# Performance work log

Hardware: AMD Instinct MI355X
Metric: run time of the kernel (lower is better)

The kernel has to match this reference:

```python
import jax, jax.numpy as jnp
import numpy as np
from jax import lax

B, C, H, W = 32, 3, 128, 128
S = 10             # max_segments
L = 200            # base_traj_length
TOTAL_LIMIT = 200  # traj_length (must equal L per original sample())
DOF = 2
HID = 2048
CONV_OUT = 512 * 6 * 6  # 128->126->63->61->30->28->14->12->6


def _conv(x, w, b):
    y = lax.conv_general_dilated(x, w, (1, 1), 'VALID', dimension_numbers=('NCHW', 'OIHW', 'NCHW'))
    return y + b[None, :, None, None]


def _pool_relu(x):
    return jax.nn.relu(lax.reduce_window(x, -jnp.inf, lax.max, (1, 1, 2, 2), (1, 1, 2, 2), 'VALID'))


def _rotate2d(y, y0, rot):
    # rotate points y (B,L,2) around per-batch center y0 (B,2) by rot (B,1,1) radians
    px, py = y[..., 0:1], y[..., 1:2]
    cx, cy = y0[:, 0][:, None, None], y0[:, 1][:, None, None]
    c, s = jnp.cos(rot), jnp.sin(rot)
    return jnp.concatenate([c * (px - cx) - s * (py - cy) + cx,
                            s * (px - cx) + c * (py - cy) + cy], axis=2)


def _sample(traj, ratio):
    b, T = traj.shape[0], traj.shape[1]
    f32 = traj.dtype
    seg_limit = jnp.ceil(ratio * TOTAL_LIMIT)  # (B,S)
    # redistribution: shave 1 off the (first) max segment while over budget.
    # original runs over_limit.max() iterations; over_limit <= S-1, extras are no-ops (still_over gate).
    for _ in range(S):
        max_val = seg_limit.max(axis=1)
        still_over = (seg_limit.sum(axis=1) != float(L)).astype(f32)
        reduced = jnp.ones((b,), f32)
        for j in range(S):
            mult = jnp.abs(jnp.sign(max_val - seg_limit[:, j]) - 1.0)
            seg_limit = seg_limit.at[:, j].add(-mult * reduced * still_over)
            reduced = jnp.clip(reduced - mult, 0.0)
    seg_ids = np.arange(T) // L
    # replicates original condition: i>0 and cur_segment_idx != floor(i - 1/L)  (note: i - 1/L, as written)
    forces = np.array([(i > 0) and (seg_ids[i] != int(np.floor(i - 1.0 / L))) for i in range(T)])
    di0 = jnp.floor((L - 1.0) / seg_limit[:, 0:1])
    init = (di0, jnp.zeros((b, 1), f32), jnp.zeros((b, 1), f32), jnp.zeros((b, S), f32))

    def step(state, inp):
        di, last_idx, n_tot, seg_cnt = state
        i_f, seg, force = inp
        lim = lax.dynamic_index_in_dim(seg_limit, seg, axis=1, keepdims=True)  # (B,1)
        cnt = lax.dynamic_index_in_dim(seg_cnt, seg, axis=1, keepdims=True)    # (B,1)
        new_di = jnp.floor((L - 1.0 - (last_idx - seg.astype(f32) * L)) / (lim - cnt))
        di = jnp.where(force | (di < new_di), new_di, di)
        chk = (jnp.sign(jnp.clip(TOTAL_LIMIT - n_tot, 0.0))
               * (cnt < lim).astype(f32)
               * (i_f - last_idx == di).astype(f32))
        last_idx = jnp.maximum(last_idx, i_f * chk)
        seg_cnt = lax.dynamic_update_index_in_dim(seg_cnt, (cnt + chk)[:, 0], seg, axis=1)
        return (di, last_idx, n_tot + chk, seg_cnt), chk[:, 0]

    xs = (jnp.arange(T, dtype=f32), jnp.asarray(seg_ids, jnp.int32), jnp.asarray(forces))
    _, mask_t = lax.scan(step, init, xs)
    mask = mask_t.T > 0  # (B,T) velocity mask; exactly TOTAL_LIMIT true per row
    idx = jnp.argsort(jnp.where(mask, 0, 1), axis=1)[:, :TOTAL_LIMIT]  # stable sort -> ordered true positions
    return jnp.take_along_axis(traj, idx[:, :, None], axis=1)


def _forward(x, w1, b1, w2, b2, w3, b3, w4, b4, fcw1, fcb1, fcw2, fcb2,
             wi, bi, ws, bs, wr, br, base_traj):
    h = _pool_relu(_conv(x, w1, b1))
    h = _pool_relu(_conv(h, w2, b2))
    h = _pool_relu(_conv(h, w3, b3))
    h = _pool_relu(_conv(h, w4, b4))
    feat = h.reshape(h.shape[0], -1)  # (B, CONV_OUT)
    z = jnp.tanh(feat @ fcw1.T + fcb1)
    z = z @ fcw2.T + fcb2             # dropout == identity (eval mode)
    init_pos = z @ wi.T + bi                                   # (B,DOF)
    seg_mod = (z @ ws.T + bs).reshape(z.shape[0], S, DOF + 1)  # (B,S,DOF+1)
    ratio = jax.nn.softmax(z @ wr.T + br, axis=1)              # (B,S)
    last_pos = init_pos[:, None, :]
    starts, segs = [last_pos], []
    for i in range(S):
        scaling = seg_mod[:, i, :-1]
        rot = jnp.tanh(seg_mod[:, i, -1])[:, None, None] * 3.14
        m = base_traj * scaling[:, None, :]
        m = _rotate2d(m, m[:, 0, :], rot)
        m = last_pos + m
        last_pos = m[:, -1:, :]
        starts.append(last_pos)
        segs.append(m)
    traj = jnp.concatenate(segs, axis=1)             # (B,S*L,DOF) unsampled
    seg_start_end = jnp.concatenate(starts, axis=1)  # (B,S+1,DOF)
    sampled = _sample(traj, ratio)                   # (B,TOTAL_LIMIT,DOF)
    return sampled, seg_start_end, ratio, traj


def setup_inputs():
    key = jax.random.key(0)
    ks = jax.random.split(key, 12)
    n = lambda k, s, sc: jax.random.normal(k, s, jnp.float32) * sc
    t = jnp.linspace(0.0, 1.0, L)
    base_traj = jnp.stack([t, jnp.sin(t * jnp.pi)], axis=-1)[None]  # (1,L,2)
    return {
        'x': n(ks[0], (B, C, H, W), 1.0),
        'w1': n(ks[1], (64, C, 3, 3), 0.05), 'b1': jnp.zeros((64,), jnp.float32),
        'w2': n(ks[2], (128, 64, 3, 3), 0.05), 'b2': jnp.zeros((128,), jnp.float32),
        'w3': n(ks[3], (256, 128, 3, 3), 0.05), 'b3': jnp.zeros((256,), jnp.float32),
        'w4': n(ks[4], (512, 256, 3, 3), 0.05), 'b4': jnp.zeros((512,), jnp.float32),
        'fcw1': n(ks[5], (HID, CONV_OUT), 0.01), 'fcb1': jnp.zeros((HID,), jnp.float32),
        'fcw2': n(ks[6], (HID, HID), 0.02), 'fcb2': jnp.zeros((HID,), jnp.float32),
        'wi': n(ks[7], (DOF, HID), 0.02), 'bi': jnp.zeros((DOF,), jnp.float32),
        'ws': n(ks[8], (S * (DOF + 1), HID), 0.02), 'bs': jnp.zeros((S * (DOF + 1),), jnp.float32),
        'wr': n(ks[9], (S, HID), 0.05), 'br': jnp.zeros((S,), jnp.float32),
        'base_traj': base_traj,
    }


def reference(x, w1, b1, w2, b2, w3, b3, w4, b4, fcw1, fcb1, fcw2, fcb2,
              wi, bi, ws, bs, wr, br, base_traj):
    return _forward(x, w1, b1, w2, b2, w3, b3, w4, b4, fcw1, fcb1, fcw2, fcb2,
                    wi, bi, ws, bs, wr, br, base_traj)
```

## Files before the change

kernel.cpp:

```cpp
#include <hip/hip_runtime.h>

__global__ __launch_bounds__(256)
void conv1_lds(const float* __restrict__ in, const float* __restrict__ wt,
               const float* __restrict__ bias, float* __restrict__ out)
{
    __shared__ float sh[3][34][34];
    int bx = blockIdx.x;
    int tile = bx & 15;
    int cg   = (bx >> 4) & 7;
    int b    = bx >> 7;
    int tr = tile >> 2, tc = tile & 3;
    int tid = threadIdx.x;
    int ty = tid >> 4, tx = tid & 15;
    int R0 = 32 * tr, C0 = 32 * tc;

    for (int t = tid; t < 3 * 34 * 34; t += 256) {
        int ci = t / 1156;
        int rem = t - ci * 1156;
        int rr = rem / 34, cc = rem - rr * 34;
        int gr = R0 + rr; if (gr > 127) gr = 127;
        int gc = C0 + cc; if (gc > 127) gc = 127;
        sh[ci][rr][cc] = in[(((size_t)b * 3 + ci) * 128 + gr) * 128 + gc];
    }
    __syncthreads();

    float acc[8][2][2] = {};
    int co0 = cg * 8;
#pragma unroll
    for (int ci = 0; ci < 3; ++ci) {
        float p[4][4];
#pragma unroll
        for (int r = 0; r < 4; ++r) {
            const float2* pr = reinterpret_cast<const float2*>(&sh[ci][2 * ty + r][2 * tx]);
            float2 a = pr[0], c2 = pr[1];
            p[r][0] = a.x; p[r][1] = a.y; p[r][2] = c2.x; p[r][3] = c2.y;
        }
#pragma unroll
        for (int j = 0; j < 8; ++j) {
            const float* wj = wt + ((size_t)(co0 + j) * 3 + ci) * 9;
#pragma unroll
            for (int kh = 0; kh < 3; ++kh)
#pragma unroll
                for (int kw = 0; kw < 3; ++kw) {
                    float wv = wj[kh * 3 + kw];
#pragma unroll
                    for (int dy = 0; dy < 2; ++dy)
#pragma unroll
                        for (int dx = 0; dx < 2; ++dx)
                            acc[j][dy][dx] = fmaf(wv, p[dy + kh][dx + kw], acc[j][dy][dx]);
                }
        }
    }
    int py = 16 * tr + ty, px = 16 * tc + tx;
    if (py < 63 && px < 63) {
#pragma unroll
        for (int j = 0; j < 8; ++j) {
            float v = fmaxf(fmaxf(acc[j][0][0], acc[j][0][1]),
                            fmaxf(acc[j][1][0], acc[j][1][1])) + bias[co0 + j];
            out[(((size_t)b * 64 + co0 + j) * 63 + py) * 63 + px] = fmaxf(v, 0.f);
        }
    }
}

template<int CIN, int DIM, int POOL, int COUT, int TILES_R, int TILES_C>
__global__ __launch_bounds__(256)
void conv_v7(const float* __restrict__ in, const float* __restrict__ wt,
             const float* __restrict__ bias, float* __restrict__ out)
{
    __shared__ __align__(16) float sh[4 * 18 * 36];
    __shared__ float wsh[16 * 37];

    constexpr int NT  = TILES_R * TILES_C;
    constexpr int NCG = COUT / 16;
    int bx = blockIdx.x;
    int tile = bx % NT;
    int cg   = (bx / NT) % NCG;
    int b    = bx / (NT * NCG);
    int rt = tile / TILES_C, ct = tile % TILES_C;
    int tid = threadIdx.x;
    int co_l = tid & 15;
    int sp   = tid >> 4;
    int ty = sp >> 2, tx = sp & 3;
    int co = cg * 16 + co_l;
    int R0 = 16 * rt, C0 = 32 * ct;

    int gofs[10], lofs[10];
#pragma unroll
    for (int j = 0; j < 10; ++j) {
        int t = tid + 256 * j; if (t > 2447) t = 2447;
        int ci = t / 612;
        int rem = t - ci * 612;
        int rr = rem / 34, cc = rem - rr * 34;
        int gr = R0 + rr; if (gr > DIM - 1) gr = DIM - 1;
        int gc = C0 + cc; if (gc > DIM - 1) gc = DIM - 1;
        gofs[j] = ci * DIM * DIM + gr * DIM + gc;
        lofs[j] = ci * 648 + rr * 36 + cc;
    }
    int wgofs[3], wlofs[3];
#pragma unroll
    for (int j = 0; j < 3; ++j) {
        int t = tid + 256 * j; if (t > 575) t = 575;
        int c = t / 36, q = t - c * 36;
        wgofs[j] = (cg * 16 + c) * CIN * 9 + q;
        wlofs[j] = c * 37 + q;
    }

    const float* gbase = in + (size_t)b * CIN * DIM * DIM;

    float acc[4][8] = {};
    float sr[10], wr[3];

#pragma unroll
    for (int j = 0; j < 10; ++j) sr[j] = gbase[gofs[j]];
#pragma unroll
    for (int j = 0; j < 3; ++j) wr[j] = wt[wgofs[j]];

    constexpr int ITERS = CIN / 4;
    for (int it = 0; it < ITERS; ++it) {
#pragma unroll
        for (int j = 0; j < 10; ++j) sh[lofs[j]] = sr[j];
#pragma unroll
        for (int j = 0; j < 3; ++j) wsh[wlofs[j]] = wr[j];
        __syncthreads();
        if (it < ITERS - 1) {
            const float* gn = gbase + (size_t)(it + 1) * 4 * DIM * DIM;
#pragma unroll
            for (int j = 0; j < 10; ++j) sr[j] = gn[gofs[j]];
            const float* wn = wt + (it + 1) * 36;
#pragma unroll
            for (int j = 0; j < 3; ++j) wr[j] = wn[wgofs[j]];
        }
#pragma unroll
        for (int ci = 0; ci < 4; ++ci) {
            float w[9];
#pragma unroll
            for (int k = 0; k < 9; ++k) w[k] = wsh[co_l * 37 + ci * 9 + k];
            const float* rb = sh + ci * 648 + 8 * tx;
#pragma unroll
            for (int r = 0; r < 6; ++r) {
                const float* rp = rb + (4 * ty + r) * 36;
                float4 a = *reinterpret_cast<const float4*>(rp);
                float4 b4 = *reinterpret_cast<const float4*>(rp + 4);
                float2 c2 = *reinterpret_cast<const float2*>(rp + 8);
                float row[10];
                row[0] = a.x;  row[1] = a.y;  row[2] = a.z;  row[3] = a.w;
                row[4] = b4.x; row[5] = b4.y; row[6] = b4.z; row[7] = b4.w;
                row[8] = c2.x; row[9] = c2.y;
#pragma unroll
                for (int y = 0; y < 4; ++y) {
                    if (y < r - 2 || y > r) continue;
                    int kh = r - y;
#pragma unroll
                    for (int kw = 0; kw < 3; ++kw) {
                        float wv = w[kh * 3 + kw];
#pragma unroll
                        for (int x = 0; x < 8; ++x)
                            acc[y][x] = fmaf(wv, row[x + kw], acc[y][x]);
                    }
                }
            }
        }
        __syncthreads();
    }
    float bz = bias[co];
#pragma unroll
    for (int dy = 0; dy < 2; ++dy) {
        int py = 8 * rt + 2 * ty + dy;
#pragma unroll
        for (int dx = 0; dx < 4; ++dx) {
            int px = 16 * ct + 4 * tx + dx;
            if (py < POOL && px < POOL) {
                float v = fmaxf(fmaxf(acc[2 * dy][2 * dx],     acc[2 * dy][2 * dx + 1]),
                                fmaxf(acc[2 * dy + 1][2 * dx], acc[2 * dy + 1][2 * dx + 1]));
                out[(((size_t)b * COUT + co) * POOL + py) * POOL + px] = fmaxf(v + bz, 0.f);
            }
        }
    }
}

__global__ __launch_bounds__(256)
void conv4_v3(const float* __restrict__ in, const float* __restrict__ wt,
              const float* __restrict__ bias, float* __restrict__ out)
{
    __shared__ __align__(16) float smem[4032 + 4 * 16 * 37];
    float* in_sh = smem;
    float* w_sh  = smem + 4032;
    float* red   = smem;

    int bx = blockIdx.x;
    int cg = bx & 31;
    int b  = bx >> 5;
    int tid = threadIdx.x;
    int h   = tid >> 6;
    int r6  = tid & 63;
    int cog = r6 >> 3;
    int sub = r6 & 7;
    int R = 3 * (sub >> 1), C = 6 * (sub & 1);

    float acc[2][3][6] = {};
    float sin_r[13];
    float sw_r[9];

    const size_t in_b = (size_t)b * 256 * 196;

#pragma unroll
    for (int j = 0; j < 13; ++j) {
        int g = tid + 256 * j;
        if (g < 3136) {
            int hh = g / 784, rem = g - hh * 784;
            int ci = rem / 196, r2 = rem - ci * 196;
            sin_r[j] = in[in_b + (size_t)(hh * 64 + ci) * 196 + r2];
        }
    }
#pragma unroll
    for (int j = 0; j < 9; ++j) {
        int g = tid + 256 * j;
        int hh = g / 576, rem = g - hh * 576;
        int co = rem / 36, q = rem - co * 36;
        sw_r[j] = wt[(size_t)(cg * 16 + co) * 2304 + (size_t)(hh * 64) * 9 + q];
    }

    for (int it = 0; it < 16; ++it) {
#pragma unroll
        for (int j = 0; j < 13; ++j) {
            int g = tid + 256 * j;
            if (g < 3136) {
                int hh = g / 784, rem = g - hh * 784;
                int ci = rem / 196, r2 = rem - ci * 196;
                int rr = r2 / 14, cc = r2 - rr * 14;
                in_sh[((hh * 4 + ci) * 14 + rr) * 18 + cc] = sin_r[j];
            }
        }
#pragma unroll
        for (int j = 0; j < 9; ++j) {
            int g = tid + 256 * j;
            int hh = g / 576, rem = g - hh * 576;
            int co = rem / 36, q = rem - co * 36;
            w_sh[(hh * 16 + co) * 37 + q] = sw_r[j];
        }
        __syncthreads();
        if (it < 15) {
            int k0n = (it + 1) * 4;
#pragma unroll
            for (int j = 0; j < 13; ++j) {
                int g = tid + 256 * j;
                if (g < 3136) {
                    int hh = g / 784, rem = g - hh * 784;
                    int ci = rem / 196, r2 = rem - ci * 196;
                    sin_r[j] = in[in_b + (size_t)(hh * 64 + k0n + ci) * 196 + r2];
                }
            }
#pragma unroll
            for (int j = 0; j < 9; ++j) {
                int g = tid + 256 * j;
                int hh = g / 576, rem = g - hh * 576;
                int co = rem / 36, q = rem - co * 36;
                sw_r[j] = wt[(size_t)(cg * 16 + co) * 2304 + (size_t)(hh * 64 + k0n) * 9 + q];
            }
        }
#pragma unroll
        for (int ci = 0; ci < 4; ++ci) {
            float w[2][9];
#pragma unroll
            for (int c = 0; c < 2; ++c)
#pragma unroll
                for (int k = 0; k < 9; ++k)
                    w[c][k] = w_sh[(h * 16 + 2 * cog + c) * 37 + ci * 9 + k];
            const float* rowbase = in_sh + ((h * 4 + ci) * 14) * 18;
#pragma unroll
            for (int r = 0; r < 5; ++r) {
                float row[8];
                const float2* pr = reinterpret_cast<const float2*>(rowbase + (size_t)(R + r) * 18 + C);
                float2 a0 = pr[0], a1 = pr[1], a2 = pr[2], a3 = pr[3];
                row[0] = a0.x; row[1] = a0.y; row[2] = a1.x; row[3] = a1.y;
                row[4] = a2.x; row[5] = a2.y; row[6] = a3.x; row[7] = a3.y;
#pragma unroll
                for (int y = 0; y < 3; ++y) {
                    if (y < r - 2 || y > r) continue;
                    int kh = r - y;
#pragma unroll
                    for (int c = 0; c < 2; ++c)
#pragma unroll
                        for (int kw = 0; kw < 3; ++kw) {
                            float wv = w[c][kh * 3 + kw];
#pragma unroll
                            for (int x = 0; x < 6; ++x)
                                acc[c][y][x] = fmaf(wv, row[x + kw], acc[c][y][x]);
                        }
                }
            }
        }
        __syncthreads();
    }
#pragma unroll
    for (int hh = 0; hh < 4; ++hh) {
        if (h == hh) {
#pragma unroll
            for (int c = 0; c < 2; ++c)
#pragma unroll
                for (int y = 0; y < 3; ++y)
#pragma unroll
                    for (int x = 0; x < 6; ++x) {
                        float* dst = &red[((2 * cog + c) * 12 + R + y) * 13 + C + x];
                        if (hh == 0) *dst = acc[c][y][x];
                        else         *dst += acc[c][y][x];
                    }
        }
        __syncthreads();
    }
    for (int t = tid; t < 576; t += 256) {
        int co = t / 36, rem = t - co * 36;
        int pr = rem / 6, pc = rem - pr * 6;
        const float* rp = &red[(co * 12 + 2 * pr) * 13 + 2 * pc];
        float v = fmaxf(fmaxf(rp[0], rp[1]), fmaxf(rp[13], rp[14]));
        v += bias[cg * 16 + co];
        out[(((size_t)b * 512 + cg * 16 + co) * 6 + pr) * 6 + pc] = fmaxf(v, 0.f);
    }
}

__global__ __launch_bounds__(1024)
void fc_big(const float* __restrict__ X, const float* __restrict__ W,
            const float* __restrict__ bias, float* __restrict__ Y,
            int K, int N, int act)
{
    __shared__ float red[32][32][8];
    int o0 = blockIdx.x * 8;
    int s = threadIdx.x & 31;
    int b = threadIdx.x >> 5;
    int K4 = K >> 2;
    const float4* X4 = reinterpret_cast<const float4*>(X) + (size_t)b * K4;
    const float4* W4 = reinterpret_cast<const float4*>(W);

    float acc[8] = {};
    for (int k4 = s; k4 < K4; k4 += 32) {
        float4 xv = X4[k4];
#pragma unroll
        for (int o = 0; o < 8; ++o) {
            float4 wv = W4[(size_t)(o0 + o) * K4 + k4];
            acc[o] = fmaf(xv.x, wv.x,
                     fmaf(xv.y, wv.y,
                     fmaf(xv.z, wv.z,
                     fmaf(xv.w, wv.w, acc[o]))));
        }
    }
#pragma unroll
    for (int o = 0; o < 8; ++o) red[b][s][o] = acc[o];
    __syncthreads();
    if (threadIdx.x < 256) {
        int bb = threadIdx.x >> 3, oo = threadIdx.x & 7;
        float v = bias[o0 + oo];
#pragma unroll 8
        for (int ss = 0; ss < 32; ++ss) v += red[bb][ss][oo];
        if (act) v = tanhf(v);
        Y[(size_t)bb * N + o0 + oo] = v;
    }
}

__global__ __launch_bounds__(256)
void fc_two(const float* __restrict__ X, const float* __restrict__ W,
            const float* __restrict__ bias, float* __restrict__ Y,
            int K, int N, int act)
{
    int o0 = blockIdx.x * 2;
    int tid = threadIdx.x;
    const float* w0 = W + (size_t)o0 * K;
    const float* w1 = w0 + K;
    float a0[32], a1[32];
#pragma unroll
    for (int b = 0; b < 32; ++b) { a0[b] = 0.f; a1[b] = 0.f; }

    for (int k = tid; k < K; k += 256) {
        float wv0 = w0[k], wv1 = w1[k];
#pragma unroll
        for (int b = 0; b < 32; ++b) {
            float xv = X[(size_t)b * K + k];
            a0[b] = fmaf(wv0, xv, a0[b]);
            a1[b] = fmaf(wv1, xv, a1[b]);
        }
    }
    __shared__ float part[2][4][32];
    int lane = tid & 63, wv = tid >> 6;
#pragma unroll
    for (int b = 0; b < 32; ++b) {
        float s0 = a0[b], s1 = a1[b];
#pragma unroll
        for (int off = 32; off >= 1; off >>= 1) {
            s0 += __shfl_down(s0, off);
            s1 += __shfl_down(s1, off);
        }
        if (lane == 0) { part[0][wv][b] = s0; part[1][wv][b] = s1; }
    }
    __syncthreads();
    if (tid < 64) {
        int j = tid >> 5, b = tid & 31;
        float s = part[j][0][b] + part[j][1][b] + part[j][2][b] + part[j][3][b] + bias[o0 + j];
        if (act) s = tanhf(s);
        Y[(size_t)b * N + o0 + j] = s;
    }
}

__global__ __launch_bounds__(64)
void post_kernel(const float* __restrict__ logits, float* __restrict__ ratio_out,
                 float* __restrict__ sl_out)
{
    int b = threadIdx.x;
    if (b >= 32) return;
    float lg[10];
#pragma unroll
    for (int j = 0; j < 10; ++j) lg[j] = logits[b * 10 + j];
    float mx = lg[0];
#pragma unroll
    for (int j = 1; j < 10; ++j) mx = fmaxf(mx, lg[j]);
    float e[10]; float ssum = 0.f;
#pragma unroll
    for (int j = 0; j < 10; ++j) { e[j] = expf(lg[j] - mx); ssum += e[j]; }
    float sl[10];
#pragma unroll
    for (int j = 0; j < 10; ++j) {
        float r = e[j] / ssum;
        ratio_out[b * 10 + j] = r;
        sl[j] = ceilf(r * 200.f);
    }
#pragma unroll
    for (int it = 0; it < 10; ++it) {
        float s = 0.f, mx2 = sl[0];
#pragma unroll
        for (int j = 0; j < 10; ++j) { s += sl[j]; mx2 = fmaxf(mx2, sl[j]); }
        float over = (s != 200.f) ? 1.f : 0.f;
        float reduced = 1.f;
#pragma unroll
        for (int j = 0; j < 10; ++j) {
            float mult = (sl[j] == mx2) ? 1.f : 0.f;
            sl[j] -= mult * reduced * over;
            reduced = fmaxf(reduced - mult, 0.f);
        }
    }
#pragma unroll
    for (int j = 0; j < 10; ++j) sl_out[b * 10 + j] = sl[j];
}

__global__ __launch_bounds__(256)
void traj_kernel(const float* __restrict__ base, const float* __restrict__ ipos,
                 const float* __restrict__ sm, float* __restrict__ out_traj,
                 float* __restrict__ out_starts)
{
    int b = blockIdx.x;
    int j = threadIdx.x;
    float bx0 = base[0], by0 = base[1];
    float bxL = base[398], byL = base[399];
    float bx = 0.f, by = 0.f;
    if (j < 200) { bx = base[2 * j]; by = base[2 * j + 1]; }
    float curx = ipos[b * 2 + 0], cury = ipos[b * 2 + 1];
    if (j == 0) { out_starts[b * 22 + 0] = curx; out_starts[b * 22 + 1] = cury; }
#pragma unroll
    for (int i = 0; i < 10; ++i) {
        float sx  = sm[b * 30 + i * 3 + 0];
        float sy  = sm[b * 30 + i * 3 + 1];
        float rot = tanhf(sm[b * 30 + i * 3 + 2]) * 3.14f;
        float c = cosf(rot), s = sinf(rot);
        float cx = bx0 * sx, cy = by0 * sy;
        if (j < 200) {
            float px = bx * sx, py = by * sy;
            float rx = c * (px - cx) - s * (py - cy) + cx;
            float ry = s * (px - cx) + c * (py - cy) + cy;
            size_t o = ((size_t)b * 2000 + i * 200 + j) * 2;
            out_traj[o + 0] = curx + rx;
            out_traj[o + 1] = cury + ry;
        }
        float pxL = bxL * sx, pyL = byL * sy;
        float exL = c * (pxL - cx) - s * (pyL - cy) + cx;
        float eyL = s * (pxL - cx) + c * (pyL - cy) + cy;
        curx += exL; cury += eyL;
        if (j == 0) {
            out_starts[b * 22 + (i + 1) * 2 + 0] = curx;
            out_starts[b * 22 + (i + 1) * 2 + 1] = cury;
        }
    }
}

__global__ __launch_bounds__(64)
void sample_kernel(const float* __restrict__ sl_in, const float* __restrict__ traj,
                   float* __restrict__ samp_out)
{
    __shared__ unsigned int maskb[32][63];
    __shared__ float ssl[32][10];
    int tid = threadIdx.x;
    for (int t = tid; t < 32 * 63; t += 64) ((unsigned int*)maskb)[t] = 0u;
    for (int t = tid; t < 32 * 10; t += 64) ((float*)ssl)[t] = sl_in[t];
    __syncthreads();
    if (tid >= 32) return;
    int b = tid;
    const float* tb = traj + (size_t)b * 4000;
    float* sp = samp_out + (size_t)b * 400;
    int out_n = 0;
    float last = 0.f, ntot = 0.f;
    float lim0 = ssl[b][0];
    float di = floorf(199.f / lim0);
    float ct0 = 0.f;
    if ((ntot < 200.f) && (ct0 < lim0) && (0.f - last == di)) {
        ntot += 1.f; ct0 += 1.f;
        maskb[b][0] |= 1u;
        sp[out_n * 2] = tb[0]; sp[out_n * 2 + 1] = tb[1]; ++out_n;
    }
    {
        float ndi = floorf((199.f - last) / (lim0 - ct0));
        if (di < ndi) di = ndi;
        if ((ntot < 200.f) && (ct0 < lim0) && (1.f - last == di)) {
            last = 1.f; ntot += 1.f; ct0 += 1.f;
            maskb[b][0] |= 2u;
            sp[out_n * 2] = tb[2]; sp[out_n * 2 + 1] = tb[3]; ++out_n;
        }
    }
    for (int seg = 0; seg < 10; ++seg) {
        float lim = ssl[b][seg];
        float ct = (seg == 0) ? ct0 : 0.f;
        float segbase = 200.f * seg;
        float segend = segbase + 199.f;
        float pos = (seg == 0) ? 2.f : segbase;
        float ndi = floorf((199.f - (last - segbase)) / (lim - ct));
        while ((ntot < 200.f) && (ct < lim)) {
            float fi = last + ndi;
            if (!(fi >= pos && fi <= segend)) break;
            int i = (int)fi;
            last = fi; ntot += 1.f; ct += 1.f;
            maskb[b][i >> 5] |= (1u << (i & 31));
            sp[out_n * 2] = tb[2 * i]; sp[out_n * 2 + 1] = tb[2 * i + 1]; ++out_n;
            pos = fi + 1.f;
            ndi = floorf((199.f - (last - segbase)) / (lim - ct));
        }
    }
    for (int i = 0; i < 2000 && out_n < 200; ++i) {
        if (!((maskb[b][i >> 5] >> (i & 31)) & 1u)) {
            sp[out_n * 2] = tb[2 * i]; sp[out_n * 2 + 1] = tb[2 * i + 1]; ++out_n;
        }
    }
}

extern "C" void kernel_launch(void* const* d_in, const int* in_sizes, int n_in,
                              void* d_out, int out_size, void* d_ws, size_t ws_size,
                              hipStream_t stream)
{
    const float* x    = (const float*)d_in[0];
    const float* w1   = (const float*)d_in[1];
    const float* b1   = (const float*)d_in[2];
    const float* w2   = (const float*)d_in[3];
    const float* b2   = (const float*)d_in[4];
    const float* w3   = (const float*)d_in[5];
    const float* b3   = (const float*)d_in[6];
    const float* w4   = (const float*)d_in[7];
    const float* b4   = (const float*)d_in[8];
    const float* fcw1 = (const float*)d_in[9];
    const float* fcb1 = (const float*)d_in[10];
    const float* fcw2 = (const float*)d_in[11];
    const float* fcb2 = (const float*)d_in[12];
    const float* wi   = (const float*)d_in[13];
    const float* bi   = (const float*)d_in[14];
    const float* wsw  = (const float*)d_in[15];
    const float* bs   = (const float*)d_in[16];
    const float* wr   = (const float*)d_in[17];
    const float* br   = (const float*)d_in[18];
    const float* base = (const float*)d_in[19];

    float* out = (float*)d_out;
    float* ws  = (float*)d_ws;

    float* p1   = ws + 0;
    float* p2   = ws + 8128512;
    float* p3   = ws + 0;
    float* feat = ws + 8128512;
    float* z1   = ws + 0;
    float* z2   = ws + 65536;
    float* ipos = ws + 131072;
    float* smod = ws + 131136;
    float* rlog = ws + 132096;
    float* slim = ws + 132416;

    float* out_samp   = out;
    float* out_starts = out + 12800;
    float* out_ratio  = out + 13504;
    float* out_traj   = out + 13824;

    conv1_lds<<<4096, 256, 0, stream>>>(x, w1, b1, p1);
    conv_v7<64, 63, 30, 128, 4, 2><<<2048, 256, 0, stream>>>(p1, w2, b2, p2);
    conv_v7<128, 30, 14, 256, 2, 1><<<1024, 256, 0, stream>>>(p2, w3, b3, p3);
    conv4_v3<<<1024, 256, 0, stream>>>(p3, w4, b4, feat);

    fc_big<<<256, 1024, 0, stream>>>(feat, fcw1, fcb1, z1, 18432, 2048, 1);
    fc_big<<<256, 1024, 0, stream>>>(z1, fcw2, fcb2, z2, 2048, 2048, 0);

    fc_two<<<1, 256, 0, stream>>>(z2, wi, bi, ipos, 2048, 2, 0);
    fc_two<<<15, 256, 0, stream>>>(z2, wsw, bs, smod, 2048, 30, 0);
    fc_two<<<5, 256, 0, stream>>>(z2, wr, br, rlog, 2048, 10, 0);

    post_kernel<<<1, 64, 0, stream>>>(rlog, out_ratio, slim);
    traj_kernel<<<32, 256, 0, stream>>>(base, ipos, smod, out_traj, out_starts);
    sample_kernel<<<1, 64, 0, stream>>>(slim, out_traj, out_samp);
}
```

Measured before the change: 989.7 us.

## Add double-buffered conv_v9 with 32 output channels per block for conv2

Measured after the change: 987.1 us. No clear change (-0.3%).

```diff
diff --git a/kernel.cpp b/kernel.cpp
--- a/kernel.cpp
+++ b/kernel.cpp
@@ -58,6 +58,135 @@
             float v = fmaxf(fmaxf(acc[j][0][0], acc[j][0][1]),
                             fmaxf(acc[j][1][0], acc[j][1][1])) + bias[co0 + j];
             out[(((size_t)b * 64 + co0 + j) * 63 + py) * 63 + px] = fmaxf(v, 0.f);
+        }
+    }
+}
+
+template<int CIN, int DIM, int POOL, int COUT, int TILES_R, int TILES_C>
+__global__ __launch_bounds__(256)
+void conv_v9(const float* __restrict__ in, const float* __restrict__ wt,
+             const float* __restrict__ bias, float* __restrict__ out)
+{
+    __shared__ __align__(16) float in_sh[2][648];
+    __shared__ __align__(16) float w_sh[2][384];
+
+    constexpr int NT  = TILES_R * TILES_C;
+    constexpr int NCG = COUT / 32;
+    int bx = blockIdx.x;
+    int tile = bx % NT;
+    int cg   = (bx / NT) % NCG;
+    int b    = bx / (NT * NCG);
+    int rt = tile / TILES_C, ct = tile % TILES_C;
+    int tid = threadIdx.x;
+    int co_l = tid & 15;
+    int sp   = tid >> 4;
+    int ty = sp >> 2, tx = sp & 3;
+    int R0 = 16 * rt, C0 = 32 * ct;
+
+    int gofs[3], lofs[3];
+#pragma unroll
+    for (int j = 0; j < 3; ++j) {
+        int t = tid + 256 * j; if (t > 611) t = 611;
+        int rr = t / 34, cc = t - rr * 34;
+        int gr = R0 + rr; if (gr > DIM - 1) gr = DIM - 1;
+        int gc = C0 + cc; if (gc > DIM - 1) gc = DIM - 1;
+        gofs[j] = gr * DIM + gc;
+        lofs[j] = rr * 36 + cc;
+    }
+    int wgofs[2], wlofs[2];
+#pragma unroll
+    for (int j = 0; j < 2; ++j) {
+        int t = tid + 256 * j; if (t > 287) t = 287;
+        int c = t / 9, k = t - c * 9;
+        wgofs[j] = (cg * 32 + c) * CIN * 9 + k;
+        wlofs[j] = c * 12 + k;
+    }
+    bool wv1 = (tid < 32);
+
+    const float* gci = in + (size_t)b * CIN * DIM * DIM;
+    const float* wci = wt;
+
+    float acc[2][4][8] = {};
+    float sr[3], wr[2];
+
+#pragma unroll
+    for (int j = 0; j < 3; ++j) sr[j] = gci[gofs[j]];
+    wr[0] = wci[wgofs[0]];
+    wr[1] = wci[wgofs[1]];
+#pragma unroll
+    for (int j = 0; j < 3; ++j) { int t = tid + 256 * j; if (t < 612) in_sh[0][lofs[j]] = sr[j]; }
+    w_sh[0][wlofs[0]] = wr[0];
+    if (wv1) w_sh[0][wlofs[1]] = wr[1];
+    __syncthreads();
+
+    for (int ci = 0; ci < CIN; ++ci) {
+        int p = ci & 1;
+        if (ci < CIN - 1) {
+            const float* gn = gci + (size_t)(ci + 1) * DIM * DIM;
+            const float* wn = wci + (size_t)(ci + 1) * 9;
+#pragma unroll
+            for (int j = 0; j < 3; ++j) sr[j] = gn[gofs[j]];
+            wr[0] = wn[wgofs[0]];
+            wr[1] = wn[wgofs[1]];
+        }
+        float w[2][9];
+#pragma unroll
+        for (int h = 0; h < 2; ++h)
+#pragma unroll
+            for (int k = 0; k < 9; ++k)
+                w[h][k] = w_sh[p][(co_l + 16 * h) * 12 + k];
+        const float* rb = in_sh[p] + 8 * tx;
+#pragma unroll
+        for (int r = 0; r < 6; ++r) {
+            const float* rp = rb + (4 * ty + r) * 36;
+            float4 a = *reinterpret_cast<const float4*>(rp);
+            float4 b4 = *reinterpret_cast<const float4*>(rp + 4);
+            float2 c2 = *reinterpret_cast<const float2*>(rp + 8);
+            float row[10];
+            row[0] = a.x;  row[1] = a.y;  row[2] = a.z;  row[3] = a.w;
+            row[4] = b4.x; row[5] = b4.y; row[6] = b4.z; row[7] = b4.w;
+            row[8] = c2.x; row[9] = c2.y;
+#pragma unroll
+            for (int y = 0; y < 4; ++y) {
+                if (y < r - 2 || y > r) continue;
+                int kh = r - y;
+#pragma unroll
+                for (int kw = 0; kw < 3; ++kw) {
+                    float w0 = w[0][kh * 3 + kw];
+                    float w1 = w[1][kh * 3 + kw];
+#pragma unroll
+                    for (int x = 0; x < 8; ++x) {
+                        acc[0][y][x] = fmaf(w0, row[x + kw], acc[0][y][x]);
+                        acc[1][y][x] = fmaf(w1, row[x + kw], acc[1][y][x]);
+                    }
+                }
+            }
+        }
+        if (ci < CIN - 1) {
+#pragma unroll
+            for (int j = 0; j < 3; ++j) { int t = tid + 256 * j; if (t < 612) in_sh[p ^ 1][lofs[j]] = sr[j]; }
+            w_sh[p ^ 1][wlofs[0]] = wr[0];
+            if (wv1) w_sh[p ^ 1][wlofs[1]] = wr[1];
+        }
+        __syncthreads();
+    }
+
+#pragma unroll
+    for (int h = 0; h < 2; ++h) {
+        int co = cg * 32 + co_l + 16 * h;
+        float bz = bias[co];
+#pragma unroll
+        for (int dy = 0; dy < 2; ++dy) {
+            int py = 8 * rt + 2 * ty + dy;
+#pragma unroll
+            for (int dx = 0; dx < 4; ++dx) {
+                int px = 16 * ct + 4 * tx + dx;
+                if (py < POOL && px < POOL) {
+                    float v = fmaxf(fmaxf(acc[h][2 * dy][2 * dx],     acc[h][2 * dy][2 * dx + 1]),
+                                    fmaxf(acc[h][2 * dy + 1][2 * dx], acc[h][2 * dy + 1][2 * dx + 1]));
+                    out[(((size_t)b * COUT + co) * POOL + py) * POOL + px] = fmaxf(v + bz, 0.f);
+                }
+            }
         }
     }
 }
@@ -581,7 +710,7 @@
     float* out_traj   = out + 13824;
 
     conv1_lds<<<4096, 256, 0, stream>>>(x, w1, b1, p1);
-    conv_v7<64, 63, 30, 128, 4, 2><<<2048, 256, 0, stream>>>(p1, w2, b2, p2);
+    conv_v9<64, 63, 30, 128, 4, 2><<<1024, 256, 0, stream>>>(p1, w2, b2, p2);
     conv_v7<128, 30, 14, 256, 2, 1><<<1024, 256, 0, stream>>>(p2, w3, b3, p3);
     conv4_v3<<<1024, 256, 0, stream>>>(p3, w4, b4, feat);
 
```

## Double output channels per thread and double-buffer per-channel input tiles in conv2/conv3

Applied to the files above, without the earlier changes.

Measured after the change: 975.2 us (median of 3 runs). About the same (-1.5%).

```diff
diff --git a/kernel.cpp b/kernel.cpp
--- a/kernel.cpp
+++ b/kernel.cpp
@@ -64,14 +64,14 @@
 
 template<int CIN, int DIM, int POOL, int COUT, int TILES_R, int TILES_C>
 __global__ __launch_bounds__(256)
-void conv_v7(const float* __restrict__ in, const float* __restrict__ wt,
+void conv_v9(const float* __restrict__ in, const float* __restrict__ wt,
              const float* __restrict__ bias, float* __restrict__ out)
 {
-    __shared__ __align__(16) float sh[4 * 18 * 36];
-    __shared__ float wsh[16 * 37];
+    __shared__ __align__(16) float in_sh[2][648];
+    __shared__ __align__(16) float w_sh[2][384];
 
     constexpr int NT  = TILES_R * TILES_C;
-    constexpr int NCG = COUT / 16;
+    constexpr int NCG = COUT / 32;
     int bx = blockIdx.x;
     int tile = bx % NT;
     int cg   = (bx / NT) % NCG;
@@ -81,98 +81,111 @@
     int co_l = tid & 15;
     int sp   = tid >> 4;
     int ty = sp >> 2, tx = sp & 3;
-    int co = cg * 16 + co_l;
     int R0 = 16 * rt, C0 = 32 * ct;
 
-    int gofs[10], lofs[10];
-#pragma unroll
-    for (int j = 0; j < 10; ++j) {
-        int t = tid + 256 * j; if (t > 2447) t = 2447;
-        int ci = t / 612;
-        int rem = t - ci * 612;
-        int rr = rem / 34, cc = rem - rr * 34;
+    int gofs[3], lofs[3];
+#pragma unroll
+    for (int j = 0; j < 3; ++j) {
+        int t = tid + 256 * j; if (t > 611) t = 611;
+        int rr = t / 34, cc = t - rr * 34;
         int gr = R0 + rr; if (gr > DIM - 1) gr = DIM - 1;
         int gc = C0 + cc; if (gc > DIM - 1) gc = DIM - 1;
-        gofs[j] = ci * DIM * DIM + gr * DIM + gc;
-        lofs[j] = ci * 648 + rr * 36 + cc;
-    }
-    int wgofs[3], wlofs[3];
-#pragma unroll
-    for (int j = 0; j < 3; ++j) {
-        int t = tid + 256 * j; if (t > 575) t = 575;
-        int c = t / 36, q = t - c * 36;
-        wgofs[j] = (cg * 16 + c) * CIN * 9 + q;
-        wlofs[j] = c * 37 + q;
-    }
-
-    const float* gbase = in + (size_t)b * CIN * DIM * DIM;
-
-    float acc[4][8] = {};
-    float sr[10], wr[3];
-
-#pragma unroll
-    for (int j = 0; j < 10; ++j) sr[j] = gbase[gofs[j]];
-#pragma unroll
-    for (int j = 0; j < 3; ++j) wr[j] = wt[wgofs[j]];
-
-    constexpr int ITERS = CIN / 4;
-    for (int it = 0; it < ITERS; ++it) {
-#pragma unroll
-        for (int j = 0; j < 10; ++j) sh[lofs[j]] = sr[j];
-#pragma unroll
-        for (int j = 0; j < 3; ++j) wsh[wlofs[j]] = wr[j];
-        __syncthreads();
-        if (it < ITERS - 1) {
-            const float* gn = gbase + (size_t)(it + 1) * 4 * DIM * DIM;
-#pragma unroll
-            for (int j = 0; j < 10; ++j) sr[j] = gn[gofs[j]];
-            const float* wn = wt + (it + 1) * 36;
-#pragma unroll
-            for (int j = 0; j < 3; ++j) wr[j] = wn[wgofs[j]];
-        }
-#pragma unroll
-        for (int ci = 0; ci < 4; ++ci) {
-            float w[9];
-#pragma unroll
-            for (int k = 0; k < 9; ++k) w[k] = wsh[co_l * 37 + ci * 9 + k];
-            const float* rb = sh + ci * 648 + 8 * tx;
-#pragma unroll
-            for (int r = 0; r < 6; ++r) {
-                const float* rp = rb + (4 * ty + r) * 36;
-                float4 a = *reinterpret_cast<const float4*>(rp);
-                float4 b4 = *reinterpret_cast<const float4*>(rp + 4);
-                float2 c2 = *reinterpret_cast<const float2*>(rp + 8);
-                float row[10];
-                row[0] = a.x;  row[1] = a.y;  row[2] = a.z;  row[3] = a.w;
-                row[4] = b4.x; row[5] = b4.y; row[6] = b4.z; row[7] = b4.w;
-                row[8] = c2.x; row[9] = c2.y;
-#pragma unroll
-                for (int y = 0; y < 4; ++y) {
-                    if (y < r - 2 || y > r) continue;
-                    int kh = r - y;
-#pragma unroll
-                    for (int kw = 0; kw < 3; ++kw) {
-                        float wv = w[kh * 3 + kw];
-#pragma unroll
-                        for (int x = 0; x < 8; ++x)
-                            acc[y][x] = fmaf(wv, row[x + kw], acc[y][x]);
+        gofs[j] = gr * DIM + gc;
+        lofs[j] = rr * 36 + cc;
+    }
+    int wgofs[2], wlofs[2];
+#pragma unroll
+    for (int j = 0; j < 2; ++j) {
+        int t = tid + 256 * j; if (t > 287) t = 287;
+        int c = t / 9, k = t - c * 9;
+        wgofs[j] = (cg * 32 + c) * CIN * 9 + k;
+        wlofs[j] = c * 12 + k;
+    }
+    bool wv1 = (tid < 32);
+
+    const float* gci = in + (size_t)b * CIN * DIM * DIM;
+    const float* wci = wt;
+
+    float acc[2][4][8] = {};
+    float sr[3], wr[2];
+
+#pragma unroll
+    for (int j = 0; j < 3; ++j) sr[j] = gci[gofs[j]];
+    wr[0] = wci[wgofs[0]];
+    wr[1] = wci[wgofs[1]];
+#pragma unroll
+    for (int j = 0; j < 3; ++j) { int t = tid + 256 * j; if (t < 612) in_sh[0][lofs[j]] = sr[j]; }
+    w_sh[0][wlofs[0]] = wr[0];
+    if (wv1) w_sh[0][wlofs[1]] = wr[1];
+    __syncthreads();
+
+    for (int ci = 0; ci < CIN; ++ci) {
+        int p = ci & 1;
+        if (ci < CIN - 1) {
+            const float* gn = gci + (size_t)(ci + 1) * DIM * DIM;
+            const float* wn = wci + (size_t)(ci + 1) * 9;
+#pragma unroll
+            for (int j = 0; j < 3; ++j) sr[j] = gn[gofs[j]];
+            wr[0] = wn[wgofs[0]];
+            wr[1] = wn[wgofs[1]];
+        }
+        float w[2][9];
+#pragma unroll
+        for (int h = 0; h < 2; ++h)
+#pragma unroll
+            for (int k = 0; k < 9; ++k)
+                w[h][k] = w_sh[p][(co_l + 16 * h) * 12 + k];
+        const float* rb = in_sh[p] + 8 * tx;
+#pragma unroll
+        for (int r = 0; r < 6; ++r) {
+            const float* rp = rb + (4 * ty + r) * 36;
+            float4 a = *reinterpret_cast<const float4*>(rp);
+            float4 b4 = *reinterpret_cast<const float4*>(rp + 4);
+            float2 c2 = *reinterpret_cast<const float2*>(rp + 8);
+            float row[10];
+            row[0] = a.x;  row[1] = a.y;  row[2] = a.z;  row[3] = a.w;
+            row[4] = b4.x; row[5] = b4.y; row[6] = b4.z; row[7] = b4.w;
+            row[8] = c2.x; row[9] = c2.y;
+#pragma unroll
+            for (int y = 0; y < 4; ++y) {
+                if (y < r - 2 || y > r) continue;
+                int kh = r - y;
+#pragma unroll
+                for (int kw = 0; kw < 3; ++kw) {
+                    float w0 = w[0][kh * 3 + kw];
+                    float w1 = w[1][kh * 3 + kw];
+#pragma unroll
+                    for (int x = 0; x < 8; ++x) {
+                        acc[0][y][x] = fmaf(w0, row[x + kw], acc[0][y][x]);
+                        acc[1][y][x] = fmaf(w1, row[x + kw], acc[1][y][x]);
                     }
                 }
             }
         }
+        if (ci < CIN - 1) {
+#pragma unroll
+            for (int j = 0; j < 3; ++j) { int t = tid + 256 * j; if (t < 612) in_sh[p ^ 1][lofs[j]] = sr[j]; }
+            w_sh[p ^ 1][wlofs[0]] = wr[0];
+            if (wv1) w_sh[p ^ 1][wlofs[1]] = wr[1];
+        }
         __syncthreads();
     }
-    float bz = bias[co];
-#pragma unroll
-    for (int dy = 0; dy < 2; ++dy) {
-        int py = 8 * rt + 2 * ty + dy;
-#pragma unroll
-        for (int dx = 0; dx < 4; ++dx) {
-            int px = 16 * ct + 4 * tx + dx;
-            if (py < POOL && px < POOL) {
-                float v = fmaxf(fmaxf(acc[2 * dy][2 * dx],     acc[2 * dy][2 * dx + 1]),
-                                fmaxf(acc[2 * dy + 1][2 * dx], acc[2 * dy + 1][2 * dx + 1]));
-                out[(((size_t)b * COUT + co) * POOL + py) * POOL + px] = fmaxf(v + bz, 0.f);
+
+#pragma unroll
+    for (int h = 0; h < 2; ++h) {
+        int co = cg * 32 + co_l + 16 * h;
+        float bz = bias[co];
+#pragma unroll
+        for (int dy = 0; dy < 2; ++dy) {
+            int py = 8 * rt + 2 * ty + dy;
+#pragma unroll
+            for (int dx = 0; dx < 4; ++dx) {
+                int px = 16 * ct + 4 * tx + dx;
+                if (py < POOL && px < POOL) {
+                    float v = fmaxf(fmaxf(acc[h][2 * dy][2 * dx],     acc[h][2 * dy][2 * dx + 1]),
+                                    fmaxf(acc[h][2 * dy + 1][2 * dx], acc[h][2 * dy + 1][2 * dx + 1]));
+                    out[(((size_t)b * COUT + co) * POOL + py) * POOL + px] = fmaxf(v + bz, 0.f);
+                }
             }
         }
     }
@@ -581,8 +594,8 @@
     float* out_traj   = out + 13824;
 
     conv1_lds<<<4096, 256, 0, stream>>>(x, w1, b1, p1);
-    conv_v7<64, 63, 30, 128, 4, 2><<<2048, 256, 0, stream>>>(p1, w2, b2, p2);
-    conv_v7<128, 30, 14, 256, 2, 1><<<1024, 256, 0, stream>>>(p2, w3, b3, p3);
+    conv_v9<64, 63, 30, 128, 4, 2><<<1024, 256, 0, stream>>>(p1, w2, b2, p2);
+    conv_v9<128, 30, 14, 256, 2, 1><<<512, 256, 0, stream>>>(p2, w3, b3, p3);
     conv4_v3<<<1024, 256, 0, stream>>>(p3, w4, b4, feat);
 
     fc_big<<<256, 1024, 0, stream>>>(feat, fcw1, fcb1, z1, 18432, 2048, 1);
```
